# Performance work log

Measured on AMD Instinct MI355X. Metric: run time of the kernel, lower is better.

## Reference

```python
import jax, jax.numpy as jnp
import numpy as np

B = 256          # batch of images
TOK = 256        # 16x16 tokens per image
V = 1024         # codebook size
D = 256          # code dim


def setup_inputs() -> dict:
    key = jax.random.key(0)
    k1, k2, k3, k4 = jax.random.split(key, 4)
    image_seq = jax.random.randint(k1, (B, TOK), 0, V, dtype=jnp.int64)
    image_seq2 = jax.random.randint(k2, (B, TOK), 0, V, dtype=jnp.int64)
    alpha = jax.random.uniform(k3, (1,), dtype=jnp.float32)
    W = jax.random.normal(k4, (V, D), dtype=jnp.float32)
    return {"image_seq": image_seq, "image_seq2": image_seq2, "alpha": alpha, "W": W}


def reference(image_seq, image_seq2, alpha, W):
    a = alpha[0]
    # gather codebook entries: [B, TOK, D]
    emb = W[image_seq]
    emb2 = W[image_seq2]
    x = (1.0 - a) * emb + a * emb2
    xf = x.reshape(-1, D)                        # [N, D], N = B*TOK
    # brute-force L2 distance to every code, without materializing [N, V, D]:
    d = (jnp.sum(xf * xf, axis=-1, keepdims=True)
         - 2.0 * xf @ W.T
         + jnp.sum(W * W, axis=-1)[None, :])
    idx = jnp.argmin(d, axis=1)                  # top-1 nearest code, [N]
    # get_codebook_entry: gather, reshape to bhwc, permute to bchw
    z_q = W[idx].reshape(B, 16, 16, D)           # [B, 16, 16, 256]
    z_q = jnp.transpose(z_q, (0, 3, 1, 2))       # [B, 256, 16, 16]
    return z_q
```

## Files before the change

kernel.cpp:

```cpp
#include <hip/hip_runtime.h>

static constexpr int Vn = 1024;
static constexpr int Dn = 256;
static constexpr int NT = 65536;

typedef float vfloat4 __attribute__((ext_vector_type(4)));

__global__ __launch_bounds__(256) void gram_kernel(const float* __restrict__ W,
                                                   float* __restrict__ G,
                                                   float* __restrict__ norms) {
    __shared__ float As[32][33];
    __shared__ float Bs[32][33];
    const int tid = threadIdx.x;
    const int tx = tid & 15;
    const int ty = tid >> 4;
    const int bm = blockIdx.y * 32;
    const int bn = blockIdx.x * 32;
    float acc[2][2] = {};
    for (int k0 = 0; k0 < Dn; k0 += 32) {
#pragma unroll
        for (int s = 0; s < 4; ++s) {
            const int e = tid + 256 * s;
            const int m = e >> 5;
            const int k = e & 31;
            As[k][m] = W[(bm + m) * Dn + k0 + k];
            Bs[k][m] = W[(bn + m) * Dn + k0 + k];
        }
        __syncthreads();
#pragma unroll
        for (int kk = 0; kk < 32; ++kk) {
            float a[2], b[2];
#pragma unroll
            for (int u = 0; u < 2; ++u) a[u] = As[kk][ty + 16 * u];
#pragma unroll
            for (int w = 0; w < 2; ++w) b[w] = Bs[kk][tx + 16 * w];
#pragma unroll
            for (int u = 0; u < 2; ++u)
#pragma unroll
                for (int w = 0; w < 2; ++w)
                    acc[u][w] = fmaf(a[u], b[w], acc[u][w]);
        }
        __syncthreads();
    }
#pragma unroll
    for (int u = 0; u < 2; ++u) {
        const int row = bm + ty + 16 * u;
#pragma unroll
        for (int w = 0; w < 2; ++w) {
            const int col = bn + tx + 16 * w;
            G[row * Vn + col] = acc[u][w];
            if (row == col) norms[row] = acc[u][w];
        }
    }
}

__global__ __launch_bounds__(256) void argmin_write_kernel(const int* __restrict__ seq,
                                                           const int* __restrict__ seq2,
                                                           const float* __restrict__ alpha,
                                                           const float* __restrict__ G,
                                                           const float* __restrict__ norms,
                                                           const float* __restrict__ W,
                                                           float* __restrict__ out) {
    __shared__ float T[32][129];
    __shared__ int bestVs[32];
    const int tid = threadIdx.x;
    const int wave = tid >> 6;
    const int lane = tid & 63;
    const int t0 = blockIdx.x * 32;

    float4 nn_r[4];
#pragma unroll
    for (int s = 0; s < 4; ++s) nn_r[s] = ((const float4*)norms)[s * 64 + lane];

    const float a = alpha[0];
    const float c0 = -2.0f * (1.0f - a);
    const float c1 = -2.0f * a;

    for (int bb = 0; bb < 2; ++bb) {
        const int base_t = t0 + wave * 8 + bb * 4;
        const int base_l = wave * 8 + bb * 4;
        int iv[4], jv[4];
#pragma unroll
        for (int q = 0; q < 4; ++q) { iv[q] = seq[base_t + q]; jv[q] = seq2[base_t + q]; }
#pragma unroll
        for (int pair = 0; pair < 2; ++pair) {
            const int qa = pair * 2, qb = pair * 2 + 1;
            const float4* GiA = (const float4*)(G + iv[qa] * Vn);
            const float4* GjA = (const float4*)(G + jv[qa] * Vn);
            const float4* GiB = (const float4*)(G + iv[qb] * Vn);
            const float4* GjB = (const float4*)(G + jv[qb] * Vn);
            float4 gia[4], gja[4], gib[4], gjb[4];
#pragma unroll
            for (int s = 0; s < 4; ++s) {
                const int e = s * 64 + lane;
                gia[s] = GiA[e];
                gja[s] = GjA[e];
                gib[s] = GiB[e];
                gjb[s] = GjB[e];
            }
            float bestA = __builtin_inff(), bestB = __builtin_inff();
            int vA = 0, vB = 0;
#pragma unroll
            for (int s = 0; s < 4; ++s) {
                const int e = s * 64 + lane;
                const float4 nn = nn_r[s];
                const int v = e * 4;
                {
                    const float s0 = fmaf(c1, gja[s].x, fmaf(c0, gia[s].x, nn.x));
                    const float s1 = fmaf(c1, gja[s].y, fmaf(c0, gia[s].y, nn.y));
                    const float s2 = fmaf(c1, gja[s].z, fmaf(c0, gia[s].z, nn.z));
                    const float s3 = fmaf(c1, gja[s].w, fmaf(c0, gia[s].w, nn.w));
                    if (s0 < bestA) { bestA = s0; vA = v; }
                    if (s1 < bestA) { bestA = s1; vA = v + 1; }
                    if (s2 < bestA) { bestA = s2; vA = v + 2; }
                    if (s3 < bestA) { bestA = s3; vA = v + 3; }
                }
                {
                    const float s0 = fmaf(c1, gjb[s].x, fmaf(c0, gib[s].x, nn.x));
                    const float s1 = fmaf(c1, gjb[s].y, fmaf(c0, gib[s].y, nn.y));
                    const float s2 = fmaf(c1, gjb[s].z, fmaf(c0, gib[s].z, nn.z));
                    const float s3 = fmaf(c1, gjb[s].w, fmaf(c0, gib[s].w, nn.w));
                    if (s0 < bestB) { bestB = s0; vB = v; }
                    if (s1 < bestB) { bestB = s1; vB = v + 1; }
                    if (s2 < bestB) { bestB = s2; vB = v + 2; }
                    if (s3 < bestB) { bestB = s3; vB = v + 3; }
                }
            }
#pragma unroll
            for (int off = 32; off >= 1; off >>= 1) {
                const float oa = __shfl_down(bestA, off, 64);
                const int   va = __shfl_down(vA, off, 64);
                if (oa < bestA || (oa == bestA && va < vA)) { bestA = oa; vA = va; }
                const float ob = __shfl_down(bestB, off, 64);
                const int   vb = __shfl_down(vB, off, 64);
                if (ob < bestB || (ob == bestB && vb < vB)) { bestB = ob; vB = vb; }
            }
            if (lane == 0) {
                bestVs[base_l + qa] = vA;
                bestVs[base_l + qb] = vB;
            }
        }
    }
    __syncthreads();

    const int b   = t0 >> 8;
    const int hw0 = t0 & 255;
    float* outb = out + b * 65536 + hw0;
    const int tok = tid >> 3;
    const int l8  = tid & 7;
    const int hw4  = (tid & 7) * 4;
    const int drow = tid >> 3;
#pragma unroll
    for (int half = 0; half < 2; ++half) {
        const int v = bestVs[tok];
        const float4* Wr = (const float4*)(W + v * Dn + half * 128);
#pragma unroll
        for (int p = 0; p < 4; ++p) {
            const int d4 = p * 8 + l8;
            const float4 w4 = Wr[d4];
            T[tok][d4 * 4 + 0] = w4.x;
            T[tok][d4 * 4 + 1] = w4.y;
            T[tok][d4 * 4 + 2] = w4.z;
            T[tok][d4 * 4 + 3] = w4.w;
        }
        __syncthreads();
#pragma unroll
        for (int dp = 0; dp < 128; dp += 32) {
            const int dl = dp + drow;
            const int d = half * 128 + dl;
            vfloat4 o;
            o.x = T[hw4 + 0][dl];
            o.y = T[hw4 + 1][dl];
            o.z = T[hw4 + 2][dl];
            o.w = T[hw4 + 3][dl];
            __builtin_nontemporal_store(o, (vfloat4*)(outb + d * 256 + hw4));
        }
        __syncthreads();
    }
}

extern "C" void kernel_launch(void* const* d_in, const int* in_sizes, int n_in,
                              void* d_out, int out_size, void* d_ws, size_t ws_size,
                              hipStream_t stream) {
    const int*   seq   = (const int*)d_in[0];
    const int*   seq2  = (const int*)d_in[1];
    const float* alpha = (const float*)d_in[2];
    const float* W     = (const float*)d_in[3];
    float* out = (float*)d_out;

    char* ws = (char*)d_ws;
    float* G     = (float*)(ws);
    float* norms = (float*)(ws + 4194304);

    gram_kernel<<<dim3(32, 32), 256, 0, stream>>>(W, G, norms);
    argmin_write_kernel<<<NT / 32, 256, 0, stream>>>(seq, seq2, alpha, G, norms, W, out);
}
```

Before: 130.4 us.

## Scan bf16 Gram rows for coarse argmin, then rescan candidates in fp32

The Gram kernel now also writes a bf16-rounded copy of the Gram matrix and a global max-abs value obtained by atomic max. The argmin kernel reads the half-size bf16 rows to find a coarse minimum per token. It then re-evaluates in exact fp32 only the codes whose coarse score falls within an error margin derived from that max. This halves the main gather bandwidth in the scan, at the cost of an extra memset, the extra bf16 writes, divergent fp32 reloads for candidates, and reliance on the error-bound margin staying correct.

```diff
diff --git a/kernel.cpp b/kernel.cpp
--- a/kernel.cpp
+++ b/kernel.cpp
@@ -8,7 +8,9 @@
 
 __global__ __launch_bounds__(256) void gram_kernel(const float* __restrict__ W,
                                                    float* __restrict__ G,
-                                                   float* __restrict__ norms) {
+                                                   unsigned short* __restrict__ Gh,
+                                                   float* __restrict__ norms,
+                                                   unsigned* __restrict__ Mg) {
     __shared__ float As[32][33];
     __shared__ float Bs[32][33];
     const int tid = threadIdx.x;
@@ -42,15 +44,58 @@
         }
         __syncthreads();
     }
+    float lmax = 0.0f;
 #pragma unroll
     for (int u = 0; u < 2; ++u) {
         const int row = bm + ty + 16 * u;
 #pragma unroll
         for (int w = 0; w < 2; ++w) {
             const int col = bn + tx + 16 * w;
-            G[row * Vn + col] = acc[u][w];
-            if (row == col) norms[row] = acc[u][w];
-        }
+            const float val = acc[u][w];
+            G[row * Vn + col] = val;
+            const unsigned b = __float_as_uint(val);
+            Gh[row * Vn + col] = (unsigned short)((b + 0x7FFFu + ((b >> 16) & 1u)) >> 16);
+            lmax = fmaxf(lmax, fabsf(val));
+            if (row == col) norms[row] = val;
+        }
+    }
+#pragma unroll
+    for (int off = 32; off >= 1; off >>= 1)
+        lmax = fmaxf(lmax, __shfl_xor(lmax, off, 64));
+    if ((tid & 63) == 0) atomicMax(Mg, __float_as_uint(lmax));
+}
+
+__device__ __forceinline__ float coarse2(unsigned u_i, unsigned u_j,
+                                         float n0, float n1,
+                                         float c0, float c1, float m) {
+    const float gi0 = __uint_as_float(u_i << 16);
+    const float gi1 = __uint_as_float(u_i & 0xFFFF0000u);
+    const float gj0 = __uint_as_float(u_j << 16);
+    const float gj1 = __uint_as_float(u_j & 0xFFFF0000u);
+    const float s0 = fmaf(c1, gj0, fmaf(c0, gi0, n0));
+    const float s1 = fmaf(c1, gj1, fmaf(c0, gi1, n1));
+    return fminf(m, fminf(s0, s1));
+}
+
+__device__ __forceinline__ void rescan2(unsigned u_i, unsigned u_j,
+                                        float n0, float n1,
+                                        float c0, float c1, float thresh, int vb,
+                                        const float* __restrict__ Gi32,
+                                        const float* __restrict__ Gj32,
+                                        float& bex, int& bv) {
+    const float gi0 = __uint_as_float(u_i << 16);
+    const float gi1 = __uint_as_float(u_i & 0xFFFF0000u);
+    const float gj0 = __uint_as_float(u_j << 16);
+    const float gj1 = __uint_as_float(u_j & 0xFFFF0000u);
+    const float s0 = fmaf(c1, gj0, fmaf(c0, gi0, n0));
+    const float s1 = fmaf(c1, gj1, fmaf(c0, gi1, n1));
+    if (s0 <= thresh) {
+        const float ex = fmaf(c1, Gj32[vb], fmaf(c0, Gi32[vb], n0));
+        if (ex < bex || (ex == bex && vb < bv)) { bex = ex; bv = vb; }
+    }
+    if (s1 <= thresh) {
+        const float ex = fmaf(c1, Gj32[vb + 1], fmaf(c0, Gi32[vb + 1], n1));
+        if (ex < bex || (ex == bex && (vb + 1) < bv)) { bex = ex; bv = vb + 1; }
     }
 }
 
@@ -58,7 +103,9 @@
                                                            const int* __restrict__ seq2,
                                                            const float* __restrict__ alpha,
                                                            const float* __restrict__ G,
+                                                           const unsigned short* __restrict__ Gh,
                                                            const float* __restrict__ norms,
+                                                           const unsigned* __restrict__ Mg,
                                                            const float* __restrict__ W,
                                                            float* __restrict__ out) {
     __shared__ float T[32][129];
@@ -69,12 +116,17 @@
     const int t0 = blockIdx.x * 32;
 
     float4 nn_r[4];
-#pragma unroll
-    for (int s = 0; s < 4; ++s) nn_r[s] = ((const float4*)norms)[s * 64 + lane];
-
+    {
+        const float4* n4 = (const float4*)norms;
+        nn_r[0] = n4[2 * lane];
+        nn_r[1] = n4[2 * lane + 1];
+        nn_r[2] = n4[128 + 2 * lane];
+        nn_r[3] = n4[129 + 2 * lane];
+    }
     const float a = alpha[0];
     const float c0 = -2.0f * (1.0f - a);
     const float c1 = -2.0f * a;
+    const float teps = __uint_as_float(*Mg) * 0.015625f;
 
     for (int bb = 0; bb < 2; ++bb) {
         const int base_t = t0 + wave * 8 + bb * 4;
@@ -85,55 +137,66 @@
 #pragma unroll
         for (int pair = 0; pair < 2; ++pair) {
             const int qa = pair * 2, qb = pair * 2 + 1;
-            const float4* GiA = (const float4*)(G + iv[qa] * Vn);
-            const float4* GjA = (const float4*)(G + jv[qa] * Vn);
-            const float4* GiB = (const float4*)(G + iv[qb] * Vn);
-            const float4* GjB = (const float4*)(G + jv[qb] * Vn);
-            float4 gia[4], gja[4], gib[4], gjb[4];
-#pragma unroll
-            for (int s = 0; s < 4; ++s) {
+            const uint4* GiA = (const uint4*)(Gh + iv[qa] * Vn);
+            const uint4* GjA = (const uint4*)(Gh + jv[qa] * Vn);
+            const uint4* GiB = (const uint4*)(Gh + iv[qb] * Vn);
+            const uint4* GjB = (const uint4*)(Gh + jv[qb] * Vn);
+            uint4 gia[2], gja[2], gib[2], gjb[2];
+#pragma unroll
+            for (int s = 0; s < 2; ++s) {
                 const int e = s * 64 + lane;
                 gia[s] = GiA[e];
                 gja[s] = GjA[e];
                 gib[s] = GiB[e];
                 gjb[s] = GjB[e];
             }
-            float bestA = __builtin_inff(), bestB = __builtin_inff();
-            int vA = 0, vB = 0;
-#pragma unroll
-            for (int s = 0; s < 4; ++s) {
-                const int e = s * 64 + lane;
-                const float4 nn = nn_r[s];
-                const int v = e * 4;
-                {
-                    const float s0 = fmaf(c1, gja[s].x, fmaf(c0, gia[s].x, nn.x));
-                    const float s1 = fmaf(c1, gja[s].y, fmaf(c0, gia[s].y, nn.y));
-                    const float s2 = fmaf(c1, gja[s].z, fmaf(c0, gia[s].z, nn.z));
-                    const float s3 = fmaf(c1, gja[s].w, fmaf(c0, gia[s].w, nn.w));
-                    if (s0 < bestA) { bestA = s0; vA = v; }
-                    if (s1 < bestA) { bestA = s1; vA = v + 1; }
-                    if (s2 < bestA) { bestA = s2; vA = v + 2; }
-                    if (s3 < bestA) { bestA = s3; vA = v + 3; }
-                }
-                {
-                    const float s0 = fmaf(c1, gjb[s].x, fmaf(c0, gib[s].x, nn.x));
-                    const float s1 = fmaf(c1, gjb[s].y, fmaf(c0, gib[s].y, nn.y));
-                    const float s2 = fmaf(c1, gjb[s].z, fmaf(c0, gib[s].z, nn.z));
-                    const float s3 = fmaf(c1, gjb[s].w, fmaf(c0, gib[s].w, nn.w));
-                    if (s0 < bestB) { bestB = s0; vB = v; }
-                    if (s1 < bestB) { bestB = s1; vB = v + 1; }
-                    if (s2 < bestB) { bestB = s2; vB = v + 2; }
-                    if (s3 < bestB) { bestB = s3; vB = v + 3; }
-                }
+            float mA = __builtin_inff(), mB = __builtin_inff();
+#pragma unroll
+            for (int s = 0; s < 2; ++s) {
+                const float4 nlo = nn_r[2 * s], nhi = nn_r[2 * s + 1];
+                mA = coarse2(gia[s].x, gja[s].x, nlo.x, nlo.y, c0, c1, mA);
+                mA = coarse2(gia[s].y, gja[s].y, nlo.z, nlo.w, c0, c1, mA);
+                mA = coarse2(gia[s].z, gja[s].z, nhi.x, nhi.y, c0, c1, mA);
+                mA = coarse2(gia[s].w, gja[s].w, nhi.z, nhi.w, c0, c1, mA);
+                mB = coarse2(gib[s].x, gjb[s].x, nlo.x, nlo.y, c0, c1, mB);
+                mB = coarse2(gib[s].y, gjb[s].y, nlo.z, nlo.w, c0, c1, mB);
+                mB = coarse2(gib[s].z, gjb[s].z, nhi.x, nhi.y, c0, c1, mB);
+                mB = coarse2(gib[s].w, gjb[s].w, nhi.z, nhi.w, c0, c1, mB);
             }
 #pragma unroll
             for (int off = 32; off >= 1; off >>= 1) {
-                const float oa = __shfl_down(bestA, off, 64);
+                mA = fminf(mA, __shfl_xor(mA, off, 64));
+                mB = fminf(mB, __shfl_xor(mB, off, 64));
+            }
+            const float thA = mA + teps;
+            const float thB = mB + teps;
+            const float* Gi32A = G + iv[qa] * Vn;
+            const float* Gj32A = G + jv[qa] * Vn;
+            const float* Gi32B = G + iv[qb] * Vn;
+            const float* Gj32B = G + jv[qb] * Vn;
+            float exA = __builtin_inff(), exB = __builtin_inff();
+            int vA = 0x7FFFFFFF, vB = 0x7FFFFFFF;
+#pragma unroll
+            for (int s = 0; s < 2; ++s) {
+                const float4 nlo = nn_r[2 * s], nhi = nn_r[2 * s + 1];
+                const int vb0 = 512 * s + 8 * lane;
+                rescan2(gia[s].x, gja[s].x, nlo.x, nlo.y, c0, c1, thA, vb0 + 0, Gi32A, Gj32A, exA, vA);
+                rescan2(gia[s].y, gja[s].y, nlo.z, nlo.w, c0, c1, thA, vb0 + 2, Gi32A, Gj32A, exA, vA);
+                rescan2(gia[s].z, gja[s].z, nhi.x, nhi.y, c0, c1, thA, vb0 + 4, Gi32A, Gj32A, exA, vA);
+                rescan2(gia[s].w, gja[s].w, nhi.z, nhi.w, c0, c1, thA, vb0 + 6, Gi32A, Gj32A, exA, vA);
+                rescan2(gib[s].x, gjb[s].x, nlo.x, nlo.y, c0, c1, thB, vb0 + 0, Gi32B, Gj32B, exB, vB);
+                rescan2(gib[s].y, gjb[s].y, nlo.z, nlo.w, c0, c1, thB, vb0 + 2, Gi32B, Gj32B, exB, vB);
+                rescan2(gib[s].z, gjb[s].z, nhi.x, nhi.y, c0, c1, thB, vb0 + 4, Gi32B, Gj32B, exB, vB);
+                rescan2(gib[s].w, gjb[s].w, nhi.z, nhi.w, c0, c1, thB, vb0 + 6, Gi32B, Gj32B, exB, vB);
+            }
+#pragma unroll
+            for (int off = 32; off >= 1; off >>= 1) {
+                const float oa = __shfl_down(exA, off, 64);
                 const int   va = __shfl_down(vA, off, 64);
-                if (oa < bestA || (oa == bestA && va < vA)) { bestA = oa; vA = va; }
-                const float ob = __shfl_down(bestB, off, 64);
+                if (oa < exA || (oa == exA && va < vA)) { exA = oa; vA = va; }
+                const float ob = __shfl_down(exB, off, 64);
                 const int   vb = __shfl_down(vB, off, 64);
-                if (ob < bestB || (ob == bestB && vb < vB)) { bestB = ob; vB = vb; }
+                if (ob < exB || (ob == exB && vb < vB)) { exB = ob; vB = vb; }
             }
             if (lane == 0) {
                 bestVs[base_l + qa] = vA;
@@ -189,9 +252,12 @@
     float* out = (float*)d_out;
 
     char* ws = (char*)d_ws;
-    float* G     = (float*)(ws);
-    float* norms = (float*)(ws + 4194304);
-
-    gram_kernel<<<dim3(32, 32), 256, 0, stream>>>(W, G, norms);
-    argmin_write_kernel<<<NT / 32, 256, 0, stream>>>(seq, seq2, alpha, G, norms, W, out);
-}
+    float*          G     = (float*)(ws);
+    float*          norms = (float*)(ws + 4194304);
+    unsigned short* Gh    = (unsigned short*)(ws + 4198400);
+    unsigned*       Mg    = (unsigned*)(ws + 6295552);
+
+    hipMemsetAsync(Mg, 0, 4, stream);
+    gram_kernel<<<dim3(32, 32), 256, 0, stream>>>(W, G, Gh, norms, Mg);
+    argmin_write_kernel<<<NT / 32, 256, 0, stream>>>(seq, seq2, alpha, G, Gh, norms, Mg, W, out);
+}
```

Result: slower. 171.7 us (+31.6%).
